# Kernel tuning notes

Measured on AMD Instinct MI355X. Metric: run time of the kernel, lower is better.

## Reference

```python
import jax, jax.numpy as jnp
import numpy as np

NHEAD = 16
FREQ = 10000.0


def rope(x, freq=FREQ):
    # x: [B, S, D]; rotary applied over the FULL feature dim (pre head-split),
    # pairing even/odd channels, matching the original module's op order.
    B, S, D = x.shape
    inv_freq = freq ** (-jnp.arange(0, D, 2, dtype=jnp.float32) / D)  # [D/2]
    ang = jnp.arange(S, dtype=jnp.float32)[:, None] * inv_freq[None, :]  # [S, D/2]
    cos, sin = jnp.cos(ang), jnp.sin(ang)
    x1, x2 = x[..., 0::2], x[..., 1::2]
    out_even = x1 * cos - x2 * sin
    out_odd = x1 * sin + x2 * cos
    return jnp.stack([out_even, out_odd], axis=-1).reshape(B, S, D)


def setup_inputs() -> dict:
    key = jax.random.key(0)
    ks = jax.random.split(key, 9)
    B, S, D = 4, 2048, 1024
    sc = 1.0 / np.sqrt(D)
    return {
        "queries": jax.random.normal(ks[0], (B, S, D), jnp.float32),
        "Wq": jax.random.normal(ks[1], (D, D), jnp.float32) * sc,
        "bq": jnp.zeros((D,), jnp.float32),
        "Wk": jax.random.normal(ks[2], (D, D), jnp.float32) * sc,
        "bk": jnp.zeros((D,), jnp.float32),
        "Wv": jax.random.normal(ks[3], (D, D), jnp.float32) * sc,
        "bv": jnp.zeros((D,), jnp.float32),
        "Wo": jax.random.normal(ks[4], (D, D), jnp.float32) * sc,
        "bo": jnp.zeros((D,), jnp.float32),
    }


def reference(queries, Wq, bq, Wk, bk, Wv, bv, Wo, bo):
    B, S, D = queries.shape
    H = NHEAD
    dh = D // H
    # self-attention: values = keys = queries
    q = rope(queries @ Wq.T + bq)
    k = rope(queries @ Wk.T + bk)
    v = queries @ Wv.T + bv
    # separate heads: [B, S, D] -> [B, H, S, dh]
    q = q.reshape(B, S, H, dh).transpose(0, 2, 1, 3)
    k = k.reshape(B, S, H, dh).transpose(0, 2, 1, 3)
    v = v.reshape(B, S, H, dh).transpose(0, 2, 1, 3)
    scores = jnp.einsum("bhqd,bhkd->bhqk", q, k) / jnp.sqrt(jnp.float32(dh))
    attn = jax.nn.softmax(scores, axis=-1)
    heads = jnp.einsum("bhqk,bhkd->bhqd", attn, v)
    out = heads.transpose(0, 2, 1, 3).reshape(B, S, D)
    return out @ Wo.T + bo
```

## Files before the change

kernel.cpp:

```cpp
#include <hip/hip_runtime.h>
#include <stdint.h>

typedef __bf16 bf16_t;
typedef __bf16 bf16x4 __attribute__((ext_vector_type(4)));
typedef __bf16 bf16x8 __attribute__((ext_vector_type(8)));
typedef float  f32x4  __attribute__((ext_vector_type(4)));

#define BB   4
#define SS   2048
#define DD   1024
#define HH   16
#define DH   64

#if __has_builtin(__builtin_amdgcn_exp2f)
#define EXP2F(x) __builtin_amdgcn_exp2f(x)
#else
#define EXP2F(x) __expf((x) * 0.6931471805599453f)
#endif

#define QSC 0.18033688011112042f

__device__ __forceinline__ void gload_lds16(const void* g, void* l) {
    __builtin_amdgcn_global_load_lds(
        (__attribute__((address_space(1))) void*)(uintptr_t)g,
        (__attribute__((address_space(3))) void*)(uint32_t)(uintptr_t)l,
        16, 0, 0);
}

__global__ __launch_bounds__(256) void prep_kernel(
        const float* __restrict__ queries,
        const float* __restrict__ Wq, const float* __restrict__ Wk,
        const float* __restrict__ Wv, const float* __restrict__ Wo,
        const float* __restrict__ bq, const float* __restrict__ bk,
        const float* __restrict__ bv,
        bf16_t* __restrict__ Xb, bf16_t* __restrict__ Wqkv,
        bf16_t* __restrict__ Wob, float* __restrict__ bqkv,
        float2* __restrict__ tab)
{
    const int bid = blockIdx.x, t = threadIdx.x;
    if (bid < 8192) {
        const int i = bid * 256 + t;
        float4 v = ((const float4*)queries)[i];
        bf16x4 o;
        o.x = (bf16_t)v.x; o.y = (bf16_t)v.y; o.z = (bf16_t)v.z; o.w = (bf16_t)v.w;
        ((bf16x4*)Xb)[i] = o;
    } else if (bid < 12288) {
        const int i = (bid - 8192) * 256 + t;
        const int which = i >> 18, p = i & 262143;
        const float* src = (which == 0) ? Wq : (which == 1) ? Wk : (which == 2) ? Wv : Wo;
        bf16_t* dst = (which < 3) ? (Wqkv + (long)which * 1048576) : Wob;
        float4 v = ((const float4*)src)[p];
        bf16x4 o;
        o.x = (bf16_t)v.x; o.y = (bf16_t)v.y; o.z = (bf16_t)v.z; o.w = (bf16_t)v.w;
        ((bf16x4*)dst)[p] = o;
    } else if (bid < 16384) {
        const int i = (bid - 12288) * 256 + t;
        const int pr = i >> 11, s = i & 2047;
        float inv = exp2f(-(float)(2 * pr) * 0.012976281620653759f);
        float c, sn;
        sincosf((float)s * inv, &sn, &c);
        tab[i] = make_float2(c, sn);
    } else {
        const int i = (bid - 16384) * 256 + t;
        if (i < 3072)
            bqkv[i] = (i < 1024) ? bq[i] : ((i < 2048) ? bk[i - 1024] : bv[i - 2048]);
    }
}

__global__ __launch_bounds__(256, 3) void gemm_qkv_rope(
        const bf16_t* __restrict__ A, const bf16_t* __restrict__ Bm,
        const float* __restrict__ bias, const float2* __restrict__ tab,
        bf16_t* __restrict__ Qb, bf16_t* __restrict__ Kb, bf16_t* __restrict__ Vt)
{
    __shared__ __attribute__((aligned(16))) bf16_t As[128 * 64];
    __shared__ __attribute__((aligned(16))) bf16_t Bs[128 * 64];
    const int t = threadIdx.x;
    const int lane = t & 63, w = t >> 6;
    const int wm = w >> 1, wn = w & 1;
    const int l15 = lane & 15, l4 = lane >> 4;
    const int xr = l15 & 7;
    const long rowA0 = (long)blockIdx.x * 128;
    const long rowB0 = (long)blockIdx.y * 128;
    const int K = 1024;

    const f32x4 vz = {0.f, 0.f, 0.f, 0.f};
    f32x4 acc[4][4];
#pragma unroll
    for (int i = 0; i < 4; ++i)
#pragma unroll
        for (int j = 0; j < 4; ++j) acc[i][j] = vz;

    int srow[4], sko[4];
#pragma unroll
    for (int i = 0; i < 4; ++i) {
        const int c = i * 256 + w * 64 + lane;
        srow[i] = c >> 3;
        sko[i]  = ((c & 7) ^ (srow[i] & 7)) << 3;
    }

    for (int kk = 0; kk < K; kk += 64) {
        __syncthreads();
#pragma unroll
        for (int i = 0; i < 4; ++i) {
            const int cb = i * 256 + w * 64;
            gload_lds16(A  + (rowA0 + srow[i]) * K + kk + sko[i], As + cb * 8);
            gload_lds16(Bm + (rowB0 + srow[i]) * K + kk + sko[i], Bs + cb * 8);
        }
        __syncthreads();
#pragma unroll
        for (int kk2 = 0; kk2 < 2; ++kk2) {
            bf16x8 af[4], bfr[4];
#pragma unroll
            for (int i = 0; i < 4; ++i)
                af[i] = *(const bf16x8*)(As + (wm * 64 + i * 16 + l15) * 64 + ((((kk2 << 2) | l4) ^ xr) * 8));
#pragma unroll
            for (int j = 0; j < 4; ++j)
                bfr[j] = *(const bf16x8*)(Bs + (wn * 64 + j * 16 + l15) * 64 + ((((kk2 << 2) | l4) ^ xr) * 8));
#pragma unroll
            for (int i = 0; i < 4; ++i)
#pragma unroll
                for (int j = 0; j < 4; ++j)
                    acc[i][j] = __builtin_amdgcn_mfma_f32_16x16x32_bf16(af[i], bfr[j], acc[i][j], 0, 0, 0);
        }
    }

    const long crow0 = rowA0 + wm * 64;
    const int  ccol0 = (int)rowB0 + wn * 64;
    const int  part  = blockIdx.y >> 3;
    const int  b     = (int)(crow0 >> 11);
    const int  s0    = (int)(crow0 & 2047);

    if (part == 2) {
        const int h = (ccol0 - 2048) >> 6;
#pragma unroll
        for (int j = 0; j < 4; ++j) {
            const int d = j * 16 + l15;
            const float bb = bias[ccol0 + j * 16 + l15];
            bf16_t* dstc = Vt + ((long)(b * HH + h) * DH + d) * SS + s0;
#pragma unroll
            for (int i = 0; i < 4; ++i) {
                bf16x4 pk;
                pk.x = (bf16_t)(acc[i][j][0] + bb);
                pk.y = (bf16_t)(acc[i][j][1] + bb);
                pk.z = (bf16_t)(acc[i][j][2] + bb);
                pk.w = (bf16_t)(acc[i][j][3] + bb);
                *(bf16x4*)(dstc + i * 16 + l4 * 4) = pk;
            }
        }
    } else {
        bf16_t* dst0 = part ? Kb : Qb;
        const float osc = part ? 1.0f : QSC;
        const int h = (ccol0 & 1023) >> 6;
        const int even = !(l15 & 1);
        bf16_t* dsth = dst0 + (long)(b * HH + h) * SS * DH;
#pragma unroll
        for (int i = 0; i < 4; ++i) {
            const int sb = s0 + i * 16 + l4 * 4;
#pragma unroll
            for (int j = 0; j < 4; ++j) {
                const int col = ccol0 + j * 16 + l15;
                const float bb = bias[col];
                const int dd = j * 16 + l15;
                const float2* trow = tab + (long)((col >> 1) & 511) * SS;
                const float4 csA = *(const float4*)(trow + sb);
                const float4 csB = *(const float4*)(trow + sb + 2);
                const float cc[4] = {csA.x, csA.z, csB.x, csB.z};
                const float sn[4] = {csA.y, csA.w, csB.y, csB.w};
#pragma unroll
                for (int r = 0; r < 4; ++r) {
                    const float val = acc[i][j][r] + bb;
                    const float par = __shfl_xor(val, 1);
                    const float out = even ? (val * cc[r] - par * sn[r])
                                           : fmaf(val, cc[r], par * sn[r]);
                    const float op = __shfl_xor(out, 1);
                    if (even) {
                        union { bf16_t hh[2]; unsigned int u; } cv;
                        cv.hh[0] = (bf16_t)(out * osc); cv.hh[1] = (bf16_t)(op * osc);
                        *(unsigned int*)(dsth + ((long)(sb + r)) * DH + dd) = cv.u;
                    }
                }
            }
        }
    }
}

template <int OUT_BF16>
__global__ __launch_bounds__(256, 3) void gemm_bt(
        const bf16_t* __restrict__ A, const bf16_t* __restrict__ Bm,
        const float* __restrict__ bias, void* __restrict__ Cout,
        int M, int N, int K)
{
    __shared__ __attribute__((aligned(16))) bf16_t As[128 * 64];
    __shared__ __attribute__((aligned(16))) bf16_t Bs[128 * 64];
    const int t = threadIdx.x;
    const int lane = t & 63, w = t >> 6;
    const int wm = w >> 1, wn = w & 1;
    const int l15 = lane & 15, l4 = lane >> 4;
    const int xr = l15 & 7;
    const long rowA0 = (long)blockIdx.x * 128;
    const long rowB0 = (long)blockIdx.y * 128;

    const f32x4 vz = {0.f, 0.f, 0.f, 0.f};
    f32x4 acc[4][4];
#pragma unroll
    for (int i = 0; i < 4; ++i)
#pragma unroll
        for (int j = 0; j < 4; ++j) acc[i][j] = vz;

    int srow[4], sko[4];
#pragma unroll
    for (int i = 0; i < 4; ++i) {
        const int c = i * 256 + w * 64 + lane;
        srow[i] = c >> 3;
        sko[i]  = ((c & 7) ^ (srow[i] & 7)) << 3;
    }

    for (int kk = 0; kk < K; kk += 64) {
        __syncthreads();
#pragma unroll
        for (int i = 0; i < 4; ++i) {
            const int cb = i * 256 + w * 64;
            gload_lds16(A  + (rowA0 + srow[i]) * K + kk + sko[i], As + cb * 8);
            gload_lds16(Bm + (rowB0 + srow[i]) * K + kk + sko[i], Bs + cb * 8);
        }
        __syncthreads();
#pragma unroll
        for (int kk2 = 0; kk2 < 2; ++kk2) {
            bf16x8 af[4], bfr[4];
#pragma unroll
            for (int i = 0; i < 4; ++i)
                af[i] = *(const bf16x8*)(As + (wm * 64 + i * 16 + l15) * 64 + ((((kk2 << 2) | l4) ^ xr) * 8));
#pragma unroll
            for (int j = 0; j < 4; ++j)
                bfr[j] = *(const bf16x8*)(Bs + (wn * 64 + j * 16 + l15) * 64 + ((((kk2 << 2) | l4) ^ xr) * 8));
#pragma unroll
            for (int i = 0; i < 4; ++i)
#pragma unroll
                for (int j = 0; j < 4; ++j)
                    acc[i][j] = __builtin_amdgcn_mfma_f32_16x16x32_bf16(af[i], bfr[j], acc[i][j], 0, 0, 0);
        }
    }

    const long crow0 = rowA0 + wm * 64;
    const int  ccol0 = (int)rowB0 + wn * 64;
#pragma unroll
    for (int i = 0; i < 4; ++i) {
#pragma unroll
        for (int j = 0; j < 4; ++j) {
            const int col = ccol0 + j * 16 + l15;
            const float bb = bias[col];
#pragma unroll
            for (int r = 0; r < 4; ++r) {
                const long row = crow0 + i * 16 + l4 * 4 + r;
                const float v = acc[i][j][r] + bb;
                if (OUT_BF16) ((bf16_t*)Cout)[row * N + col] = (bf16_t)v;
                else          ((float*)Cout)[row * N + col]  = v;
            }
        }
    }
}

__global__ __launch_bounds__(512, 4) void attn_kernel(const bf16_t* __restrict__ Qb,
                                                      const bf16_t* __restrict__ Kb,
                                                      const bf16_t* __restrict__ Vt,
                                                      bf16_t* __restrict__ Ob)
{
    __shared__ __attribute__((aligned(16))) bf16_t Ks[64 * 64];
    __shared__ __attribute__((aligned(16))) bf16_t Vs[64 * 64];
    __shared__ __attribute__((aligned(16))) bf16_t Ps[256 * 72];
    const int t = threadIdx.x, lane = t & 63, w = t >> 6;
    const int l15 = lane & 15, l4 = lane >> 4;
    const int xr = l15 & 7;
    const int bh = blockIdx.x, qt = blockIdx.y;
    const bf16_t* Qbh = Qb + (long)bh * SS * DH;
    const bf16_t* Kbh = Kb + (long)bh * SS * DH;
    const bf16_t* Vbh = Vt + (long)bh * DH * SS;

    const int qbase = qt * 256 + w * 32;
    bf16x8 qf[2][2];
#pragma unroll
    for (int s = 0; s < 2; ++s) {
        const long qrow = qbase + 16 * s + l15;
        qf[s][0] = *(const bf16x8*)(Qbh + qrow * DH + l4 * 8);
        qf[s][1] = *(const bf16x8*)(Qbh + qrow * DH + 32 + l4 * 8);
    }

    bf16x8 ones;
#pragma unroll
    for (int e = 0; e < 8; ++e) ones[e] = (bf16_t)1.0f;

    const f32x4 vz = {0.f, 0.f, 0.f, 0.f};
    f32x4 oacc[2][4];
    f32x4 lacc[2];
#pragma unroll
    for (int s = 0; s < 2; ++s) {
        lacc[s] = vz;
#pragma unroll
        for (int j = 0; j < 4; ++j) oacc[s][j] = vz;
    }

    const int L    = w * 64 + lane;
    const int srow = L >> 3;
    const int scc  = (L & 7) ^ (srow & 7);

    for (int kt = 0; kt < SS / 64; ++kt) {
        __syncthreads();
        const bf16_t* Ksrc = Kbh + (long)kt * 64 * DH;
        gload_lds16(Ksrc + srow * 64 + scc * 8, Ks + L * 8);
        gload_lds16(Vbh + (long)srow * SS + kt * 64 + scc * 8, Vs + L * 8);
        __syncthreads();

        f32x4 sacc[2][4];
#pragma unroll
        for (int s = 0; s < 2; ++s)
#pragma unroll
            for (int j = 0; j < 4; ++j) sacc[s][j] = vz;
#pragma unroll
        for (int j = 0; j < 4; ++j) {
            const int rk = (j * 16 + l15) * 64;
            const bf16x8 kf0 = *(const bf16x8*)(Ks + rk + ((l4 ^ xr) * 8));
            const bf16x8 kf1 = *(const bf16x8*)(Ks + rk + (((4 + l4) ^ xr) * 8));
#pragma unroll
            for (int s = 0; s < 2; ++s) {
                sacc[s][j] = __builtin_amdgcn_mfma_f32_16x16x32_bf16(kf0, qf[s][0], sacc[s][j], 0, 0, 0);
                sacc[s][j] = __builtin_amdgcn_mfma_f32_16x16x32_bf16(kf1, qf[s][1], sacc[s][j], 0, 0, 0);
            }
        }

#pragma unroll
        for (int s = 0; s < 2; ++s) {
#pragma unroll
            for (int j = 0; j < 4; ++j) {
                const float p0 = EXP2F(sacc[s][j][0]);
                const float p1 = EXP2F(sacc[s][j][1]);
                const float p2 = EXP2F(sacc[s][j][2]);
                const float p3 = EXP2F(sacc[s][j][3]);
                bf16x4 pk;
                pk.x = (bf16_t)p0; pk.y = (bf16_t)p1; pk.z = (bf16_t)p2; pk.w = (bf16_t)p3;
                *(bf16x4*)(Ps + (w * 32 + 16 * s + l15) * 72 + j * 16 + l4 * 4) = pk;
            }
        }

        bf16x8 pf[2][2];
#pragma unroll
        for (int s = 0; s < 2; ++s) {
            pf[s][0] = *(const bf16x8*)(Ps + (w * 32 + 16 * s + l15) * 72 + l4 * 8);
            pf[s][1] = *(const bf16x8*)(Ps + (w * 32 + 16 * s + l15) * 72 + 32 + l4 * 8);
            lacc[s] = __builtin_amdgcn_mfma_f32_16x16x32_bf16(pf[s][0], ones, lacc[s], 0, 0, 0);
            lacc[s] = __builtin_amdgcn_mfma_f32_16x16x32_bf16(pf[s][1], ones, lacc[s], 0, 0, 0);
        }
#pragma unroll
        for (int j = 0; j < 4; ++j) {
            const int rv = (j * 16 + l15) * 64;
            const bf16x8 vf0 = *(const bf16x8*)(Vs + rv + ((l4 ^ xr) * 8));
            const bf16x8 vf1 = *(const bf16x8*)(Vs + rv + (((4 + l4) ^ xr) * 8));
#pragma unroll
            for (int s = 0; s < 2; ++s) {
                oacc[s][j] = __builtin_amdgcn_mfma_f32_16x16x32_bf16(pf[s][0], vf0, oacc[s][j], 0, 0, 0);
                oacc[s][j] = __builtin_amdgcn_mfma_f32_16x16x32_bf16(pf[s][1], vf1, oacc[s][j], 0, 0, 0);
            }
        }
    }

    const int b = bh >> 4, h = bh & 15;
#pragma unroll
    for (int s = 0; s < 2; ++s) {
        float invr[4];
#pragma unroll
        for (int r = 0; r < 4; ++r)
            invr[r] = 1.0f / lacc[s][r];
#pragma unroll
        for (int j = 0; j < 4; ++j) {
#pragma unroll
            for (int r = 0; r < 4; ++r) {
                const int row = qbase + 16 * s + l4 * 4 + r;
                const float v = oacc[s][j][r] * invr[r];
                Ob[((long)(b * SS + row)) * DD + h * DH + j * 16 + l15] = (bf16_t)v;
            }
        }
    }
}

extern "C" void kernel_launch(void* const* d_in, const int* in_sizes, int n_in,
                              void* d_out, int out_size, void* d_ws, size_t ws_size,
                              hipStream_t stream)
{
    const float* queries = (const float*)d_in[0];
    const float* Wq = (const float*)d_in[1];
    const float* bq = (const float*)d_in[2];
    const float* Wk = (const float*)d_in[3];
    const float* bk = (const float*)d_in[4];
    const float* Wv = (const float*)d_in[5];
    const float* bv = (const float*)d_in[6];
    const float* Wo = (const float*)d_in[7];
    const float* bo = (const float*)d_in[8];

    char* ws = (char*)d_ws;
    size_t off = 0;
    auto alloc = [&](size_t bytes) { size_t o = off; off += (bytes + 255) & ~(size_t)255; return o; };
    bf16_t* Xb   = (bf16_t*)(ws + alloc(8192u * 1024u * 2u));
    bf16_t* Wqkv = (bf16_t*)(ws + alloc(3072u * 1024u * 2u));
    bf16_t* Wob  = (bf16_t*)(ws + alloc(1024u * 1024u * 2u));
    float*  bqkv = (float*) (ws + alloc(3072u * 4u));
    float2* tab  = (float2*)(ws + alloc(2048u * 512u * 8u));
    bf16_t* Qb   = (bf16_t*)(ws + alloc(64u * 2048u * 64u * 2u));
    bf16_t* Kb   = (bf16_t*)(ws + alloc(64u * 2048u * 64u * 2u));
    bf16_t* Vt   = (bf16_t*)(ws + alloc(64u * 64u * 2048u * 2u));
    bf16_t* Ob   = Xb;

    prep_kernel<<<16396, 256, 0, stream>>>(queries, Wq, Wk, Wv, Wo, bq, bk, bv,
                                           Xb, Wqkv, Wob, bqkv, tab);

    gemm_qkv_rope<<<dim3(64, 24), 256, 0, stream>>>(Xb, Wqkv, bqkv, tab, Qb, Kb, Vt);
    attn_kernel<<<dim3(64, 8), 512, 0, stream>>>(Qb, Kb, Vt, Ob);
    gemm_bt<0><<<dim3(64, 8), 256, 0, stream>>>(Ob, Wob, bo, d_out, 8192, 1024, 1024);
}
```

Before: 259.3 us.

## Double-buffer K/V tiles in attention to overlap loads with compute

The attention kernel's K and V shared-memory tiles become two buffers each. The next tile's global-to-LDS load is issued right after the barrier, so it can overlap the MFMA work on the current tile, and the old post-load sync is removed. An explicit barrier at the end of each iteration keeps the buffer being refilled from being overwritten while other waves still read it. This doubles the K/V LDS footprint, which may cut resident blocks per CU. The overlap also depends on the compiler not inserting a conservative vmcnt wait before the LDS reads.

Result: slower. 274.8 us (+6.0%).

```diff
diff --git a/kernel.cpp b/kernel.cpp
--- a/kernel.cpp
+++ b/kernel.cpp
@@ -265,8 +265,8 @@
                                                       const bf16_t* __restrict__ Vt,
                                                       bf16_t* __restrict__ Ob)
 {
-    __shared__ __attribute__((aligned(16))) bf16_t Ks[64 * 64];
-    __shared__ __attribute__((aligned(16))) bf16_t Vs[64 * 64];
+    __shared__ __attribute__((aligned(16))) bf16_t Ks[2][64 * 64];
+    __shared__ __attribute__((aligned(16))) bf16_t Vs[2][64 * 64];
     __shared__ __attribute__((aligned(16))) bf16_t Ps[256 * 72];
     const int t = threadIdx.x, lane = t & 63, w = t >> 6;
     const int l15 = lane & 15, l4 = lane >> 4;
@@ -302,13 +302,22 @@
     const int L    = w * 64 + lane;
     const int srow = L >> 3;
     const int scc  = (L & 7) ^ (srow & 7);
-
-    for (int kt = 0; kt < SS / 64; ++kt) {
+    const int NT   = SS / 64;
+
+    auto stage = [&](int b, int kt2) {
+        const bf16_t* Ksrc = Kbh + (long)kt2 * 64 * DH;
+        gload_lds16(Ksrc + srow * 64 + scc * 8, Ks[b] + L * 8);
+        gload_lds16(Vbh + (long)srow * SS + kt2 * 64 + scc * 8, Vs[b] + L * 8);
+    };
+
+    stage(0, 0);
+
+    for (int kt = 0; kt < NT; ++kt) {
+        const int cur = kt & 1;
         __syncthreads();
-        const bf16_t* Ksrc = Kbh + (long)kt * 64 * DH;
-        gload_lds16(Ksrc + srow * 64 + scc * 8, Ks + L * 8);
-        gload_lds16(Vbh + (long)srow * SS + kt * 64 + scc * 8, Vs + L * 8);
-        __syncthreads();
+        if (kt + 1 < NT) stage(cur ^ 1, kt + 1);
+        const bf16_t* Ksb = Ks[cur];
+        const bf16_t* Vsb = Vs[cur];
 
         f32x4 sacc[2][4];
 #pragma unroll
@@ -318,8 +327,8 @@
 #pragma unroll
         for (int j = 0; j < 4; ++j) {
             const int rk = (j * 16 + l15) * 64;
-            const bf16x8 kf0 = *(const bf16x8*)(Ks + rk + ((l4 ^ xr) * 8));
-            const bf16x8 kf1 = *(const bf16x8*)(Ks + rk + (((4 + l4) ^ xr) * 8));
+            const bf16x8 kf0 = *(const bf16x8*)(Ksb + rk + ((l4 ^ xr) * 8));
+            const bf16x8 kf1 = *(const bf16x8*)(Ksb + rk + (((4 + l4) ^ xr) * 8));
 #pragma unroll
             for (int s = 0; s < 2; ++s) {
                 sacc[s][j] = __builtin_amdgcn_mfma_f32_16x16x32_bf16(kf0, qf[s][0], sacc[s][j], 0, 0, 0);
@@ -352,14 +361,16 @@
 #pragma unroll
         for (int j = 0; j < 4; ++j) {
             const int rv = (j * 16 + l15) * 64;
-            const bf16x8 vf0 = *(const bf16x8*)(Vs + rv + ((l4 ^ xr) * 8));
-            const bf16x8 vf1 = *(const bf16x8*)(Vs + rv + (((4 + l4) ^ xr) * 8));
+            const bf16x8 vf0 = *(const bf16x8*)(Vsb + rv + ((l4 ^ xr) * 8));
+            const bf16x8 vf1 = *(const bf16x8*)(Vsb + rv + (((4 + l4) ^ xr) * 8));
 #pragma unroll
             for (int s = 0; s < 2; ++s) {
                 oacc[s][j] = __builtin_amdgcn_mfma_f32_16x16x32_bf16(pf[s][0], vf0, oacc[s][j], 0, 0, 0);
                 oacc[s][j] = __builtin_amdgcn_mfma_f32_16x16x32_bf16(pf[s][1], vf1, oacc[s][j], 0, 0, 0);
             }
         }
+
+        __builtin_amdgcn_s_barrier();
     }
 
     const int b = bh >> 4, h = bh & 15;
```
